# Performance work log

Hardware: AMD Instinct MI355X
Metric: run time of the kernel (lower is better)

## Reference

```python
import jax, jax.numpy as jnp
import numpy as np

N_NODES = 50000
N_EDGES = 800000
IN_CH = 512
HID = 256
HEADS = 8
OUT_CH = 64


def _glorot(key, shape):
    fan_in = shape[0] if len(shape) == 2 else shape[-1]
    return jax.random.normal(key, shape, jnp.float32) / jnp.sqrt(jnp.float32(fan_in))


def setup_inputs() -> dict:
    key = jax.random.key(0)
    ks = jax.random.split(key, 16)
    C = HID // HEADS  # 32, per-head dim
    return {
        "x": jax.random.normal(ks[0], (N_NODES, IN_CH), jnp.float32),
        "edge_index": jax.random.randint(ks[1], (2, N_EDGES), 0, N_NODES, jnp.int32),
        # layer 0: in -> heads*C, concat
        "W0": _glorot(ks[2], (IN_CH, HEADS * C)),
        "a_src0": _glorot(ks[3], (HEADS, C)),
        "a_dst0": _glorot(ks[4], (HEADS, C)),
        "b0": jnp.zeros((HEADS * C,), jnp.float32),
        # layer 1: hidden -> heads*C, concat
        "W1": _glorot(ks[5], (HID, HEADS * C)),
        "a_src1": _glorot(ks[6], (HEADS, C)),
        "a_dst1": _glorot(ks[7], (HEADS, C)),
        "b1": jnp.zeros((HEADS * C,), jnp.float32),
        # layer 2: hidden -> out_ch, 1 head, mean (concat=False)
        "W2": _glorot(ks[8], (HID, 1 * OUT_CH)),
        "a_src2": _glorot(ks[9], (1, OUT_CH)),
        "a_dst2": _glorot(ks[10], (1, OUT_CH)),
        "b2": jnp.zeros((OUT_CH,), jnp.float32),
    }


def gat_conv(x, W, a_src, a_dst, b, src, dst, concat):
    """PyG GATConv (self-loops already appended to src/dst), eval mode."""
    N = x.shape[0]
    H, C = a_src.shape
    h = (x @ W).reshape(N, H, C)                      # [N,H,C]
    alpha_src = jnp.sum(h * a_src, axis=-1)           # [N,H]
    alpha_dst = jnp.sum(h * a_dst, axis=-1)           # [N,H]
    e = jax.nn.leaky_relu(alpha_src[src] + alpha_dst[dst], 0.2)  # [E,H]
    # softmax over incoming edges per destination node
    m = jax.ops.segment_max(e, dst, num_segments=N)   # [N,H]
    m = jnp.where(jnp.isfinite(m), m, 0.0)
    w = jnp.exp(e - m[dst])
    s = jax.ops.segment_sum(w, dst, num_segments=N)
    alpha = w / (s[dst] + 1e-16)                      # [E,H]
    out = jax.ops.segment_sum(alpha[:, :, None] * h[src], dst, num_segments=N)
    out = out.reshape(N, H * C) if concat else out.mean(axis=1)
    return out + b


def reference(x, edge_index, W0, a_src0, a_dst0, b0, W1, a_src1, a_dst1, b1, W2, a_src2, a_dst2, b2):
    N = x.shape[0]
    loop = jnp.arange(N, dtype=edge_index.dtype)      # add_self_loops=True
    src = jnp.concatenate([edge_index[0], loop])
    dst = jnp.concatenate([edge_index[1], loop])
    # dropout is identity in eval mode
    h = jax.nn.elu(gat_conv(x, W0, a_src0, a_dst0, b0, src, dst, True))
    h = jax.nn.elu(gat_conv(h, W1, a_src1, a_dst1, b1, src, dst, True))
    h = gat_conv(h, W2, a_src2, a_dst2, b2, src, dst, False)
    return jax.nn.log_softmax(h, axis=1)
```

## Files before the change

kernel.cpp:

```cpp
#include <hip/hip_runtime.h>
#include <hip/hip_bf16.h>

typedef __attribute__((ext_vector_type(8))) short short8;
typedef __attribute__((ext_vector_type(4))) float f32x4;
typedef __attribute__((ext_vector_type(2))) float f32x2;
typedef __attribute__((ext_vector_type(4))) unsigned short us4;

__device__ __forceinline__ ushort f2bf(float f) {
    unsigned u = __float_as_uint(f);
    u += 0x7FFFu + ((u >> 16) & 1u);
    return (ushort)(u >> 16);
}
__device__ __forceinline__ float bf2f(ushort h) {
    return __uint_as_float(((unsigned)h) << 16);
}
__device__ __forceinline__ float lrelu(float e) { return (e >= 0.f) ? e : 0.2f * e; }
__device__ __forceinline__ unsigned char f2fp8(float v) {
    return (unsigned char)(__builtin_amdgcn_cvt_pk_fp8_f32(v, v, 0, false) & 0xFF);
}
__device__ __forceinline__ void gload16(const void* g, void* l) {
    __builtin_amdgcn_global_load_lds(
        (const __attribute__((address_space(1))) unsigned int*)g,
        (__attribute__((address_space(3))) unsigned int*)l, 16, 0, 0);
}

__global__ void k_hist(const int* __restrict__ dst, int* __restrict__ deg, int e) {
    int i = blockIdx.x * blockDim.x + threadIdx.x;
    if (i < e) atomicAdd(&deg[dst[i]], 1);
}
__global__ void k_scanA(const int* __restrict__ deg, int* __restrict__ bsum, int n) {
    __shared__ int sd[256];
    int t = blockIdx.x * 256 + threadIdx.x;
    sd[threadIdx.x] = (t < n) ? deg[t] + 1 : 0;
    __syncthreads();
    for (int off = 128; off > 0; off >>= 1) {
        if (threadIdx.x < off) sd[threadIdx.x] += sd[threadIdx.x + off];
        __syncthreads();
    }
    if (threadIdx.x == 0) bsum[blockIdx.x] = sd[0];
}
__global__ void k_scanC(const int* __restrict__ deg, const int* __restrict__ bsum,
                        int* __restrict__ rowptr, int* __restrict__ cursor,
                        int n, int etot, int nb) {
    __shared__ int sb[256];
    __shared__ int sd[256];
    __shared__ int sbx[256];
    int i = threadIdx.x;
    int bv = (i < nb) ? bsum[i] : 0;
    sb[i] = bv;
    __syncthreads();
    for (int off = 1; off < 256; off <<= 1) {
        int tv = (i >= off) ? sb[i - off] : 0;
        __syncthreads();
        sb[i] += tv;
        __syncthreads();
    }
    sbx[i] = sb[i] - bv;
    __syncthreads();
    int boff = sbx[blockIdx.x];

    int t = blockIdx.x * 256 + i;
    int v = (t < n) ? deg[t] + 1 : 0;
    sd[i] = v;
    __syncthreads();
    for (int off = 1; off < 256; off <<= 1) {
        int tv = (i >= off) ? sd[i - off] : 0;
        __syncthreads();
        sd[i] += tv;
        __syncthreads();
    }
    if (t < n) {
        int ex = boff + sd[i] - v;
        rowptr[t] = ex;
        cursor[t] = ex;
        if (t == n - 1) rowptr[n] = etot;
    }
}
__global__ void k_scatter(const int* __restrict__ ei, int* __restrict__ cursor,
                          int* __restrict__ col, int e, int n) {
    int i = blockIdx.x * blockDim.x + threadIdx.x;
    int etot = e + n;
    if (i >= etot) return;
    int s, d;
    if (i < e) { s = ei[i]; d = ei[e + i]; }
    else       { s = i - e; d = s; }
    int pos = atomicAdd(&cursor[d], 1);
    col[pos] = s;
}

__global__ void k_wcvt3(const float* __restrict__ W0, ushort* __restrict__ T0,
                        const float* __restrict__ W1, ushort* __restrict__ T1,
                        const float* __restrict__ W2, ushort* __restrict__ T2,
                        int* __restrict__ deg, int n) {
    int i = blockIdx.x * blockDim.x + threadIdx.x;
    if (i < n) deg[i] = 0;
    if (i < 131072) {
        int k = i >> 8, c = i & 255;
        T0[(size_t)c * 512 + k] = f2bf(W0[i]);
    } else if (i < 196608) {
        int j = i - 131072;
        int k = j >> 8, c = j & 255;
        T1[(size_t)c * 256 + k] = f2bf(W1[j]);
    } else if (i < 212992) {
        int j = i - 196608;
        int k = j >> 6, c = j & 63;
        T2[(size_t)c * 256 + k] = f2bf(W2[j]);
    }
}

template <int K, int BN, bool AF32>
__global__ __launch_bounds__(256) void k_gemm(const void* __restrict__ Ap,
                                              const ushort* __restrict__ BT,
                                              unsigned char* __restrict__ Cp,
                                              const float* __restrict__ asv,
                                              const float* __restrict__ adv,
                                              float* __restrict__ asrc,
                                              float* __restrict__ adst, int M) {
    constexpr int BM = 64, BK = 32;
    constexpr int NK = K / BK;
    constexpr int NF = BN / 32;
    constexpr int AU = BM * BK / 8;
    constexpr int BU = BN * BK / 8;
    constexpr int TU = AU + BU;
    __shared__ __align__(16) ushort lds[2][TU * 8];

    const int t = threadIdx.x;
    const int wid = t >> 6, lane = t & 63;
    const int lr = lane & 15, lg = lane >> 4;
    const int wm = wid >> 1, wn = wid & 1;
    const int bm0 = blockIdx.x * BM;
    const int bn0 = blockIdx.y * BN;
    const int Nc = BN * gridDim.y;

    int a_off[2], b_off[NF];
#pragma unroll
    for (int mf = 0; mf < 2; ++mf) {
        int row = wm * 32 + mf * 16 + lr;
        a_off[mf] = row * 64 + ((lg ^ ((row >> 1) & 3)) << 4);
    }
#pragma unroll
    for (int nf = 0; nf < NF; ++nf) {
        int col = wn * (BN / 2) + nf * 16 + lr;
        b_off[nf] = AU * 16 + col * 64 + ((lg ^ ((col >> 1) & 3)) << 4);
    }

    f32x4 acc[2][NF];
#pragma unroll
    for (int mf = 0; mf < 2; ++mf)
#pragma unroll
        for (int nf = 0; nf < NF; ++nf) acc[mf][nf] = f32x4{0.f, 0.f, 0.f, 0.f};

    f32x4 ra[2];

    auto stage_B = [&](int buf, int kk) {
#pragma unroll
        for (int i = 0; i < 2; ++i) {
            int u = t + i * 256;
            int col = u >> 2;
            int g = (u & 3) ^ ((col >> 1) & 3);
            const ushort* src = BT + (size_t)(bn0 + col) * K + kk + g * 8;
            gload16(src, &lds[buf][(AU + u) * 8]);
        }
    };
    auto stage_A16 = [&](int buf, int kk) {
        int u = t;
        int row = u >> 2;
        int g = (u & 3) ^ ((row >> 1) & 3);
        int grow = bm0 + row;
        if (grow >= M) grow = M - 1;
        const ushort* src = (const ushort*)Ap + (size_t)grow * K + kk + g * 8;
        gload16(src, &lds[buf][u * 8]);
    };
    auto load_A32 = [&](int kk) {
        int u = t;
        int row = u >> 2;
        int g = (u & 3) ^ ((row >> 1) & 3);
        int grow = bm0 + row;
        if (grow >= M) grow = M - 1;
        const float* src = (const float*)Ap + (size_t)grow * K + kk + g * 8;
        ra[0] = *(const f32x4*)src;
        ra[1] = *(const f32x4*)(src + 4);
    };
    auto write_A32 = [&](int buf) {
        int u = t;
        short8 v;
#pragma unroll
        for (int j = 0; j < 4; ++j) {
            v[j] = (short)f2bf(ra[0][j]);
            v[4 + j] = (short)f2bf(ra[1][j]);
        }
        *(short8*)&lds[buf][u * 8] = v;
    };
    auto compute = [&](int buf) {
        const char* base = (const char*)lds[buf];
        short8 af[2], bf_[NF];
#pragma unroll
        for (int mf = 0; mf < 2; ++mf) af[mf] = *(const short8*)(base + a_off[mf]);
#pragma unroll
        for (int nf = 0; nf < NF; ++nf) bf_[nf] = *(const short8*)(base + b_off[nf]);
#pragma unroll
        for (int mf = 0; mf < 2; ++mf)
#pragma unroll
            for (int nf = 0; nf < NF; ++nf)
                acc[mf][nf] = __builtin_amdgcn_mfma_f32_16x16x32_bf16(af[mf], bf_[nf], acc[mf][nf], 0, 0, 0);
    };

    if constexpr (AF32) {
        load_A32(0);
        write_A32(0);
    } else {
        stage_A16(0, 0);
    }
    stage_B(0, 0);
    __syncthreads();

    int buf = 0;
    for (int ks = 0; ks < NK; ++ks) {
        const int kk = (ks + 1) * BK;
        if (ks + 1 < NK) {
            if constexpr (AF32) load_A32(kk);
            else stage_A16(buf ^ 1, kk);
            stage_B(buf ^ 1, kk);
        }
        compute(buf);
        if constexpr (AF32) {
            if (ks + 1 < NK) write_A32(buf ^ 1);
        }
        __syncthreads();
        buf ^= 1;
    }

#pragma unroll
    for (int mf = 0; mf < 2; ++mf) {
#pragma unroll
        for (int nf = 0; nf < NF; ++nf) {
            int col = bn0 + wn * (BN / 2) + nf * 16 + lr;
#pragma unroll
            for (int p = 0; p < 4; ++p) {
                int row = bm0 + wm * 32 + mf * 16 + lg * 4 + p;
                if (row < M)
                    Cp[(size_t)row * Nc + col] = f2fp8(acc[mf][nf][p]);
            }
        }
    }

    if constexpr (NF == 4) {
        float cs[4], cd[4];
#pragma unroll
        for (int nf = 0; nf < 4; ++nf) {
            int col = bn0 + wn * 64 + nf * 16 + lr;
            cs[nf] = asv[col];
            cd[nf] = adv[col];
        }
        const int hb = (bn0 >> 5) + wn * 2;
#pragma unroll
        for (int mf = 0; mf < 2; ++mf) {
#pragma unroll
            for (int p = 0; p < 4; ++p) {
                float sA = acc[mf][0][p] * cs[0] + acc[mf][1][p] * cs[1];
                float sB = acc[mf][2][p] * cs[2] + acc[mf][3][p] * cs[3];
                float dA = acc[mf][0][p] * cd[0] + acc[mf][1][p] * cd[1];
                float dB = acc[mf][2][p] * cd[2] + acc[mf][3][p] * cd[3];
#pragma unroll
                for (int off = 1; off < 16; off <<= 1) {
                    sA += __shfl_xor(sA, off);
                    sB += __shfl_xor(sB, off);
                    dA += __shfl_xor(dA, off);
                    dB += __shfl_xor(dB, off);
                }
                int row = bm0 + wm * 32 + mf * 16 + lg * 4 + p;
                if (lr == 0 && row < M) {
                    asrc[row * 8 + hb] = sA;
                    asrc[row * 8 + hb + 1] = sB;
                    adst[row * 8 + hb] = dA;
                    adst[row * 8 + hb + 1] = dB;
                }
            }
        }
    }
}

__global__ __launch_bounds__(256) void k_gemm2(const ushort* __restrict__ Ap,
                                               const ushort* __restrict__ BT,
                                               ushort* __restrict__ Cp,
                                               const float* __restrict__ asv,
                                               const float* __restrict__ adv,
                                               float* __restrict__ asrc,
                                               float* __restrict__ adst, int M) {
    constexpr int K = 256, BM = 64, BK = 32;
    constexpr int NK = K / BK;
    constexpr int BU = 64 * BK / 8;
    constexpr int AU = BM * BK / 8;
    constexpr int TU = AU + BU;
    __shared__ __align__(16) ushort lds[2][TU * 8];

    const int t = threadIdx.x;
    const int wid = t >> 6, lane = t & 63;
    const int lr = lane & 15, lg = lane >> 4;
    const int bm0 = blockIdx.x * BM;

    int a_off0, b_off[4];
    {
        int row = wid * 16 + lr;
        a_off0 = row * 64 + ((lg ^ ((row >> 1) & 3)) << 4);
    }
#pragma unroll
    for (int nf = 0; nf < 4; ++nf) {
        int col = nf * 16 + lr;
        b_off[nf] = AU * 16 + col * 64 + ((lg ^ ((col >> 1) & 3)) << 4);
    }

    f32x4 acc[4];
#pragma unroll
    for (int nf = 0; nf < 4; ++nf) acc[nf] = f32x4{0.f, 0.f, 0.f, 0.f};

    auto stage_B = [&](int buf, int kk) {
        int u = t;
        int col = u >> 2;
        int g = (u & 3) ^ ((col >> 1) & 3);
        const ushort* src = BT + (size_t)col * K + kk + g * 8;
        gload16(src, &lds[buf][(AU + u) * 8]);
    };
    auto stage_A = [&](int buf, int kk) {
        int u = t;
        int row = u >> 2;
        int g = (u & 3) ^ ((row >> 1) & 3);
        int grow = bm0 + row;
        if (grow >= M) grow = M - 1;
        const ushort* src = Ap + (size_t)grow * K + kk + g * 8;
        gload16(src, &lds[buf][u * 8]);
    };
    auto compute = [&](int buf) {
        const char* base = (const char*)lds[buf];
        short8 af = *(const short8*)(base + a_off0);
        short8 bf_[4];
#pragma unroll
        for (int nf = 0; nf < 4; ++nf) bf_[nf] = *(const short8*)(base + b_off[nf]);
#pragma unroll
        for (int nf = 0; nf < 4; ++nf)
            acc[nf] = __builtin_amdgcn_mfma_f32_16x16x32_bf16(af, bf_[nf], acc[nf], 0, 0, 0);
    };

    stage_A(0, 0);
    stage_B(0, 0);
    __syncthreads();
    int buf = 0;
    for (int ks = 0; ks < NK; ++ks) {
        if (ks + 1 < NK) {
            stage_A(buf ^ 1, (ks + 1) * BK);
            stage_B(buf ^ 1, (ks + 1) * BK);
        }
        compute(buf);
        __syncthreads();
        buf ^= 1;
    }

    float cs[4], cd[4];
#pragma unroll
    for (int nf = 0; nf < 4; ++nf) {
        cs[nf] = asv[nf * 16 + lr];
        cd[nf] = adv[nf * 16 + lr];
    }
#pragma unroll
    for (int p = 0; p < 4; ++p) {
        int row = bm0 + wid * 16 + lg * 4 + p;
#pragma unroll
        for (int nf = 0; nf < 4; ++nf) {
            if (row < M)
                Cp[(size_t)row * 64 + nf * 16 + lr] = f2bf(acc[nf][p]);
        }
        float sA = acc[0][p] * cs[0] + acc[1][p] * cs[1] +
                   acc[2][p] * cs[2] + acc[3][p] * cs[3];
        float dA = acc[0][p] * cd[0] + acc[1][p] * cd[1] +
                   acc[2][p] * cd[2] + acc[3][p] * cd[3];
#pragma unroll
        for (int off = 1; off < 16; off <<= 1) {
            sA += __shfl_xor(sA, off);
            dA += __shfl_xor(dA, off);
        }
        if (lr == 0 && row < M) {
            asrc[row] = sA;
            adst[row] = dA;
        }
    }
}

#define MAXW 96
__global__ __launch_bounds__(128) void k_agg(const unsigned char* __restrict__ h8,
                                             const float* __restrict__ asrc,
                                             const float* __restrict__ adst,
                                             const int* __restrict__ rowptr,
                                             const int* __restrict__ col,
                                             const float* __restrict__ bias,
                                             ushort* __restrict__ anext, int n) {
    __shared__ float wl[2][MAXW * 8];
    int wid = threadIdx.x >> 6;
    int lane = threadIdx.x & 63;
    int node = blockIdx.x * 2 + wid;
    if (node >= n) return;
    int beg = rowptr[node], end = rowptr[node + 1];
    int deg = end - beg;
    int hd = lane >> 3;
    int eo = lane & 7;
    float ad = adst[node * 8 + hd];
    float* wp = wl[wid];

    float sacc = 0.f;
    for (int jb = eo; jb < deg; jb += 8) {
        int s = col[beg + jb];
        float w = __expf(lrelu(asrc[s * 8 + hd] + ad));
        if (jb < MAXW) wp[jb * 8 + hd] = w;
        sacc += w;
    }
    sacc += __shfl_xor(sacc, 1);
    sacc += __shfl_xor(sacc, 2);
    sacc += __shfl_xor(sacc, 4);
    float inv = 1.f / (sacc + 1e-16f);

    int nl = (deg < MAXW) ? deg : MAXW;
    float a0 = 0.f, a1 = 0.f, a2 = 0.f, a3 = 0.f;
    int jb = 0;
    for (; jb + 8 <= nl; jb += 8) {
        int sv[8];
#pragma unroll
        for (int i = 0; i < 8; ++i) sv[i] = col[beg + jb + i];
        unsigned gv[8];
#pragma unroll
        for (int i = 0; i < 8; ++i) gv[i] = *(const unsigned*)(h8 + (size_t)sv[i] * 256 + lane * 4);
        float wv[8];
#pragma unroll
        for (int i = 0; i < 8; ++i) wv[i] = wp[(jb + i) * 8 + hd];
#pragma unroll
        for (int i = 0; i < 8; ++i) {
            a0 += wv[i] * __builtin_amdgcn_cvt_f32_fp8(gv[i], 0);
            a1 += wv[i] * __builtin_amdgcn_cvt_f32_fp8(gv[i], 1);
            a2 += wv[i] * __builtin_amdgcn_cvt_f32_fp8(gv[i], 2);
            a3 += wv[i] * __builtin_amdgcn_cvt_f32_fp8(gv[i], 3);
        }
    }
    for (; jb < nl; ++jb) {
        int s = col[beg + jb];
        unsigned g = *(const unsigned*)(h8 + (size_t)s * 256 + lane * 4);
        float w = wp[jb * 8 + hd];
        a0 += w * __builtin_amdgcn_cvt_f32_fp8(g, 0);
        a1 += w * __builtin_amdgcn_cvt_f32_fp8(g, 1);
        a2 += w * __builtin_amdgcn_cvt_f32_fp8(g, 2);
        a3 += w * __builtin_amdgcn_cvt_f32_fp8(g, 3);
    }
    for (; jb < deg; ++jb) {
        int s = col[beg + jb];
        unsigned g = *(const unsigned*)(h8 + (size_t)s * 256 + lane * 4);
        float w = __expf(lrelu(asrc[s * 8 + hd] + ad));
        a0 += w * __builtin_amdgcn_cvt_f32_fp8(g, 0);
        a1 += w * __builtin_amdgcn_cvt_f32_fp8(g, 1);
        a2 += w * __builtin_amdgcn_cvt_f32_fp8(g, 2);
        a3 += w * __builtin_amdgcn_cvt_f32_fp8(g, 3);
    }
    f32x4 bv = *(const f32x4*)(bias + lane * 4);
    float v0 = a0 * inv + bv[0];
    float v1 = a1 * inv + bv[1];
    float v2 = a2 * inv + bv[2];
    float v3 = a3 * inv + bv[3];
    v0 = (v0 > 0.f) ? v0 : expm1f(v0);
    v1 = (v1 > 0.f) ? v1 : expm1f(v1);
    v2 = (v2 > 0.f) ? v2 : expm1f(v2);
    v3 = (v3 > 0.f) ? v3 : expm1f(v3);
    us4 o;
    o[0] = f2bf(v0); o[1] = f2bf(v1); o[2] = f2bf(v2); o[3] = f2bf(v3);
    *(us4*)(anext + (size_t)node * 256 + lane * 4) = o;
}

__global__ __launch_bounds__(128) void k_agg2(const ushort* __restrict__ h2,
                                              const float* __restrict__ asrc,
                                              const float* __restrict__ adst,
                                              const int* __restrict__ rowptr,
                                              const int* __restrict__ col,
                                              const float* __restrict__ bias,
                                              float* __restrict__ out, int n) {
    int wid = threadIdx.x >> 6;
    int lane = threadIdx.x & 63;
    int node = blockIdx.x * 2 + wid;
    if (node >= n) return;
    int beg = rowptr[node], end = rowptr[node + 1];
    int deg = end - beg;
    float ad = adst[node];
    int g = lane >> 3;
    int ch = (lane & 7) * 8;

    f32x2 acc2[4];
#pragma unroll
    for (int i = 0; i < 4; ++i) acc2[i] = f32x2{0.f, 0.f};
    float ssum = 0.f;
    for (int p = 0; p < deg; p += 8) {
        int jb = p + g;
        float w = 0.f;
        uint4 gv = {0u, 0u, 0u, 0u};
        if (jb < deg) {
            int s = col[beg + jb];
            gv = *(const uint4*)(h2 + (size_t)s * 64 + ch);
            w = __expf(lrelu(asrc[s] + ad));
        }
        ssum += w;
        f32x2 w2 = {w, w};
        f32x2 p0 = {__uint_as_float(gv.x << 16), __uint_as_float(gv.x & 0xFFFF0000u)};
        f32x2 p1 = {__uint_as_float(gv.y << 16), __uint_as_float(gv.y & 0xFFFF0000u)};
        f32x2 p2 = {__uint_as_float(gv.z << 16), __uint_as_float(gv.z & 0xFFFF0000u)};
        f32x2 p3 = {__uint_as_float(gv.w << 16), __uint_as_float(gv.w & 0xFFFF0000u)};
        acc2[0] += w2 * p0;
        acc2[1] += w2 * p1;
        acc2[2] += w2 * p2;
        acc2[3] += w2 * p3;
    }
    float v[8];
#pragma unroll
    for (int i = 0; i < 4; ++i) { v[2 * i] = acc2[i].x; v[2 * i + 1] = acc2[i].y; }
#pragma unroll
    for (int off = 8; off < 64; off <<= 1) {
        ssum += __shfl_xor(ssum, off);
#pragma unroll
        for (int i = 0; i < 8; ++i) v[i] += __shfl_xor(v[i], off);
    }
    float inv = 1.f / (ssum + 1e-16f);
#pragma unroll
    for (int i = 0; i < 8; ++i) v[i] = v[i] * inv + bias[ch + i];
    float mx = v[0];
#pragma unroll
    for (int i = 1; i < 8; ++i) mx = fmaxf(mx, v[i]);
    mx = fmaxf(mx, __shfl_xor(mx, 1));
    mx = fmaxf(mx, __shfl_xor(mx, 2));
    mx = fmaxf(mx, __shfl_xor(mx, 4));
    float se = 0.f;
#pragma unroll
    for (int i = 0; i < 8; ++i) se += __expf(v[i] - mx);
    se += __shfl_xor(se, 1);
    se += __shfl_xor(se, 2);
    se += __shfl_xor(se, 4);
    float ls = mx + logf(se);
    if (g == 0) {
        f32x4 o0, o1;
#pragma unroll
        for (int i = 0; i < 4; ++i) { o0[i] = v[i] - ls; o1[i] = v[4 + i] - ls; }
        *(f32x4*)(out + (size_t)node * 64 + ch) = o0;
        *(f32x4*)(out + (size_t)node * 64 + ch + 4) = o1;
    }
}

extern "C" void kernel_launch(void* const* d_in, const int* in_sizes, int n_in,
                              void* d_out, int out_size, void* d_ws, size_t ws_size,
                              hipStream_t stream) {
    const float* x   = (const float*)d_in[0];
    const int*   ei  = (const int*)d_in[1];
    const float* W0  = (const float*)d_in[2];
    const float* as0 = (const float*)d_in[3];
    const float* ad0 = (const float*)d_in[4];
    const float* b0  = (const float*)d_in[5];
    const float* W1  = (const float*)d_in[6];
    const float* as1 = (const float*)d_in[7];
    const float* ad1 = (const float*)d_in[8];
    const float* b1  = (const float*)d_in[9];
    const float* W2  = (const float*)d_in[10];
    const float* as2 = (const float*)d_in[11];
    const float* ad2 = (const float*)d_in[12];
    const float* b2  = (const float*)d_in[13];
    float* out = (float*)d_out;

    const int N = in_sizes[0] / 512;
    const int E = in_sizes[1] / 2;
    const int ETOT = E + N;

    char* ws = (char*)d_ws;
    size_t off = 0;
    auto alloc = [&](size_t bytes) -> void* {
        off = (off + 255) & ~(size_t)255;
        void* p = ws + off;
        off += bytes;
        return p;
    };
    int* rowptr = (int*)alloc((size_t)(N + 1) * 4);
    int* cursor = (int*)alloc((size_t)N * 4);
    int* deg    = (int*)alloc((size_t)N * 4);
    int* bsum   = (int*)alloc(1024);
    int* colb   = (int*)alloc((size_t)ETOT * 4);
    ushort* WT0 = (ushort*)alloc((size_t)256 * 512 * 2);
    ushort* WT1 = (ushort*)alloc((size_t)256 * 256 * 2);
    ushort* WT2 = (ushort*)alloc((size_t)64 * 256 * 2);
    unsigned char* h8 = (unsigned char*)alloc((size_t)N * 256);
    ushort* abf = (ushort*)alloc((size_t)N * 256 * 2);
    float* asrc = (float*)alloc((size_t)N * 8 * 4);
    float* adst = (float*)alloc((size_t)N * 8 * 4);
    ushort* h2   = (ushort*)h8;
    float* asrc2 = asrc;
    float* adst2 = adst;

    const int nblk = (N + 255) / 256;

    k_wcvt3<<<832, 256, 0, stream>>>(W0, WT0, W1, WT1, W2, WT2, deg, N);

    k_hist<<<(E + 255) / 256, 256, 0, stream>>>(ei + E, deg, E);
    k_scanA<<<nblk, 256, 0, stream>>>(deg, bsum, N);
    k_scanC<<<nblk, 256, 0, stream>>>(deg, bsum, rowptr, cursor, N, ETOT, nblk);
    k_scatter<<<(ETOT + 255) / 256, 256, 0, stream>>>(ei, cursor, colb, E, N);

    const dim3 g01((N + 63) / 64, 2);
    const int gblk = (N + 63) / 64;
    const int ablk = (N + 1) / 2;

    k_gemm<512, 128, true><<<g01, 256, 0, stream>>>(x, WT0, h8, as0, ad0, asrc, adst, N);
    k_agg<<<ablk, 128, 0, stream>>>(h8, asrc, adst, rowptr, colb, b0, abf, N);

    k_gemm<256, 128, false><<<g01, 256, 0, stream>>>(abf, WT1, h8, as1, ad1, asrc, adst, N);
    k_agg<<<ablk, 128, 0, stream>>>(h8, asrc, adst, rowptr, colb, b1, abf, N);

    k_gemm2<<<gblk, 256, 0, stream>>>(abf, WT2, h2, as2, ad2, asrc2, adst2, N);
    k_agg2<<<ablk, 128, 0, stream>>>(h2, asrc2, adst2, rowptr, colb, b2, out, N);
}
```

Baseline: 325.0 us.

## Fuse degree histogram into weight conversion and CSR scatter into layer-0 GEMM

Merges the edge degree histogram into the weight-transpose kernel as extra blocks, and runs the CSR column scatter as extra blocks inside the layer-0 GEMM launch. Each of those blocks now handles four edges. The degree buffer is cleared with a memset instead of inside the conversion kernel. This removes two kernel launches and lets the scatter's atomics overlap with GEMM work, but adds a memset call and puts atomic-heavy blocks alongside MFMA blocks in one grid.

New measurement: 328.4 us. Within noise of the previous version (+1.0%).

```diff
diff --git a/kernel.cpp b/kernel.cpp
--- a/kernel.cpp
+++ b/kernel.cpp
@@ -24,10 +24,6 @@
         (__attribute__((address_space(3))) unsigned int*)l, 16, 0, 0);
 }
 
-__global__ void k_hist(const int* __restrict__ dst, int* __restrict__ deg, int e) {
-    int i = blockIdx.x * blockDim.x + threadIdx.x;
-    if (i < e) atomicAdd(&deg[dst[i]], 1);
-}
 __global__ void k_scanA(const int* __restrict__ deg, int* __restrict__ bsum, int n) {
     __shared__ int sd[256];
     int t = blockIdx.x * 256 + threadIdx.x;
@@ -76,24 +72,23 @@
         if (t == n - 1) rowptr[n] = etot;
     }
 }
-__global__ void k_scatter(const int* __restrict__ ei, int* __restrict__ cursor,
-                          int* __restrict__ col, int e, int n) {
+
+__global__ void k_wh(const float* __restrict__ W0, ushort* __restrict__ T0,
+                     const float* __restrict__ W1, ushort* __restrict__ T1,
+                     const float* __restrict__ W2, ushort* __restrict__ T2,
+                     const int* __restrict__ dst, int* __restrict__ deg, int e, int nhb) {
+    if (blockIdx.x >= 832) {
+        int hb = blockIdx.x - 832;
+        int base = hb * 256 + threadIdx.x;
+        int stride = nhb * 256;
+#pragma unroll
+        for (int k = 0; k < 4; ++k) {
+            int i = base + k * stride;
+            if (i < e) atomicAdd(&deg[dst[i]], 1);
+        }
+        return;
+    }
     int i = blockIdx.x * blockDim.x + threadIdx.x;
-    int etot = e + n;
-    if (i >= etot) return;
-    int s, d;
-    if (i < e) { s = ei[i]; d = ei[e + i]; }
-    else       { s = i - e; d = s; }
-    int pos = atomicAdd(&cursor[d], 1);
-    col[pos] = s;
-}
-
-__global__ void k_wcvt3(const float* __restrict__ W0, ushort* __restrict__ T0,
-                        const float* __restrict__ W1, ushort* __restrict__ T1,
-                        const float* __restrict__ W2, ushort* __restrict__ T2,
-                        int* __restrict__ deg, int n) {
-    int i = blockIdx.x * blockDim.x + threadIdx.x;
-    if (i < n) deg[i] = 0;
     if (i < 131072) {
         int k = i >> 8, c = i & 255;
         T0[(size_t)c * 512 + k] = f2bf(W0[i]);
@@ -108,8 +103,181 @@
     }
 }
 
-template <int K, int BN, bool AF32>
-__global__ __launch_bounds__(256) void k_gemm(const void* __restrict__ Ap,
+__global__ __launch_bounds__(256) void k_g0s(const float* __restrict__ Ap,
+                                             const ushort* __restrict__ BT,
+                                             unsigned char* __restrict__ Cp,
+                                             const float* __restrict__ asv,
+                                             const float* __restrict__ adv,
+                                             float* __restrict__ asrc,
+                                             float* __restrict__ adst, int M,
+                                             const int* __restrict__ ei,
+                                             int* __restrict__ cursor,
+                                             int* __restrict__ colb,
+                                             int E, int nsb) {
+    constexpr int K = 512, BK = 32;
+    constexpr int NK = K / BK;
+    constexpr int AU = 256, BU = 512, TU = AU + BU;
+    __shared__ __align__(16) ushort lds[2][TU * 8];
+
+    if (blockIdx.x < nsb) {
+        int base = blockIdx.x * 256 + threadIdx.x;
+        int stride = nsb * 256;
+        int etot = E + M;
+#pragma unroll
+        for (int k = 0; k < 4; ++k) {
+            int i = base + k * stride;
+            if (i < etot) {
+                int s, d;
+                if (i < E) { s = ei[i]; d = ei[E + i]; }
+                else       { s = i - E; d = s; }
+                int pos = atomicAdd(&cursor[d], 1);
+                colb[pos] = s;
+            }
+        }
+        return;
+    }
+
+    const int gb = blockIdx.x - nsb;
+    const int t = threadIdx.x;
+    const int wid = t >> 6, lane = t & 63;
+    const int lr = lane & 15, lg = lane >> 4;
+    const int wm = wid >> 1, wn = wid & 1;
+    const int bm0 = (gb >> 1) * 64;
+    const int bn0 = (gb & 1) * 128;
+
+    int a_off[2], b_off[4];
+#pragma unroll
+    for (int mf = 0; mf < 2; ++mf) {
+        int row = wm * 32 + mf * 16 + lr;
+        a_off[mf] = row * 64 + ((lg ^ ((row >> 1) & 3)) << 4);
+    }
+#pragma unroll
+    for (int nf = 0; nf < 4; ++nf) {
+        int col = wn * 64 + nf * 16 + lr;
+        b_off[nf] = AU * 16 + col * 64 + ((lg ^ ((col >> 1) & 3)) << 4);
+    }
+
+    f32x4 acc[2][4];
+#pragma unroll
+    for (int mf = 0; mf < 2; ++mf)
+#pragma unroll
+        for (int nf = 0; nf < 4; ++nf) acc[mf][nf] = f32x4{0.f, 0.f, 0.f, 0.f};
+
+    f32x4 ra[2];
+
+    auto stage_B = [&](int buf, int kk) {
+#pragma unroll
+        for (int i = 0; i < 2; ++i) {
+            int u = t + i * 256;
+            int col = u >> 2;
+            int g = (u & 3) ^ ((col >> 1) & 3);
+            const ushort* src = BT + (size_t)(bn0 + col) * K + kk + g * 8;
+            gload16(src, &lds[buf][(AU + u) * 8]);
+        }
+    };
+    auto load_A32 = [&](int kk) {
+        int u = t;
+        int row = u >> 2;
+        int g = (u & 3) ^ ((row >> 1) & 3);
+        int grow = bm0 + row;
+        if (grow >= M) grow = M - 1;
+        const float* src = Ap + (size_t)grow * K + kk + g * 8;
+        ra[0] = *(const f32x4*)src;
+        ra[1] = *(const f32x4*)(src + 4);
+    };
+    auto write_A32 = [&](int buf) {
+        short8 v;
+#pragma unroll
+        for (int j = 0; j < 4; ++j) {
+            v[j] = (short)f2bf(ra[0][j]);
+            v[4 + j] = (short)f2bf(ra[1][j]);
+        }
+        *(short8*)&lds[buf][t * 8] = v;
+    };
+    auto compute = [&](int buf) {
+        const char* base = (const char*)lds[buf];
+        short8 af[2], bf_[4];
+#pragma unroll
+        for (int mf = 0; mf < 2; ++mf) af[mf] = *(const short8*)(base + a_off[mf]);
+#pragma unroll
+        for (int nf = 0; nf < 4; ++nf) bf_[nf] = *(const short8*)(base + b_off[nf]);
+#pragma unroll
+        for (int mf = 0; mf < 2; ++mf)
+#pragma unroll
+            for (int nf = 0; nf < 4; ++nf)
+                acc[mf][nf] = __builtin_amdgcn_mfma_f32_16x16x32_bf16(af[mf], bf_[nf], acc[mf][nf], 0, 0, 0);
+    };
+
+    load_A32(0);
+    write_A32(0);
+    stage_B(0, 0);
+    __syncthreads();
+
+    int buf = 0;
+    for (int ks = 0; ks < NK; ++ks) {
+        const int kk = (ks + 1) * BK;
+        if (ks + 1 < NK) {
+            load_A32(kk);
+            stage_B(buf ^ 1, kk);
+        }
+        compute(buf);
+        if (ks + 1 < NK) write_A32(buf ^ 1);
+        __syncthreads();
+        buf ^= 1;
+    }
+
+#pragma unroll
+    for (int mf = 0; mf < 2; ++mf) {
+#pragma unroll
+        for (int nf = 0; nf < 4; ++nf) {
+            int col = bn0 + wn * 64 + nf * 16 + lr;
+#pragma unroll
+            for (int p = 0; p < 4; ++p) {
+                int row = bm0 + wm * 32 + mf * 16 + lg * 4 + p;
+                if (row < M)
+                    Cp[(size_t)row * 256 + col] = f2fp8(acc[mf][nf][p]);
+            }
+        }
+    }
+
+    {
+        float cs[4], cd[4];
+#pragma unroll
+        for (int nf = 0; nf < 4; ++nf) {
+            int col = bn0 + wn * 64 + nf * 16 + lr;
+            cs[nf] = asv[col];
+            cd[nf] = adv[col];
+        }
+        const int hb = (bn0 >> 5) + wn * 2;
+#pragma unroll
+        for (int mf = 0; mf < 2; ++mf) {
+#pragma unroll
+            for (int p = 0; p < 4; ++p) {
+                float sA = acc[mf][0][p] * cs[0] + acc[mf][1][p] * cs[1];
+                float sB = acc[mf][2][p] * cs[2] + acc[mf][3][p] * cs[3];
+                float dA = acc[mf][0][p] * cd[0] + acc[mf][1][p] * cd[1];
+                float dB = acc[mf][2][p] * cd[2] + acc[mf][3][p] * cd[3];
+#pragma unroll
+                for (int off = 1; off < 16; off <<= 1) {
+                    sA += __shfl_xor(sA, off);
+                    sB += __shfl_xor(sB, off);
+                    dA += __shfl_xor(dA, off);
+                    dB += __shfl_xor(dB, off);
+                }
+                int row = bm0 + wm * 32 + mf * 16 + lg * 4 + p;
+                if (lr == 0 && row < M) {
+                    asrc[row * 8 + hb] = sA;
+                    asrc[row * 8 + hb + 1] = sB;
+                    adst[row * 8 + hb] = dA;
+                    adst[row * 8 + hb + 1] = dB;
+                }
+            }
+        }
+    }
+}
+
+template <int K, int BN>
+__global__ __launch_bounds__(256) void k_gemm(const ushort* __restrict__ Ap,
                                               const ushort* __restrict__ BT,
                                               unsigned char* __restrict__ Cp,
                                               const float* __restrict__ asv,
@@ -150,8 +318,6 @@
 #pragma unroll
         for (int nf = 0; nf < NF; ++nf) acc[mf][nf] = f32x4{0.f, 0.f, 0.f, 0.f};
 
-    f32x4 ra[2];
-
     auto stage_B = [&](int buf, int kk) {
 #pragma unroll
         for (int i = 0; i < 2; ++i) {
@@ -168,28 +334,8 @@
         int g = (u & 3) ^ ((row >> 1) & 3);
         int grow = bm0 + row;
         if (grow >= M) grow = M - 1;
-        const ushort* src = (const ushort*)Ap + (size_t)grow * K + kk + g * 8;
+        const ushort* src = Ap + (size_t)grow * K + kk + g * 8;
         gload16(src, &lds[buf][u * 8]);
-    };
-    auto load_A32 = [&](int kk) {
-        int u = t;
-        int row = u >> 2;
-        int g = (u & 3) ^ ((row >> 1) & 3);
-        int grow = bm0 + row;
-        if (grow >= M) grow = M - 1;
-        const float* src = (const float*)Ap + (size_t)grow * K + kk + g * 8;
-        ra[0] = *(const f32x4*)src;
-        ra[1] = *(const f32x4*)(src + 4);
-    };
-    auto write_A32 = [&](int buf) {
-        int u = t;
-        short8 v;
-#pragma unroll
-        for (int j = 0; j < 4; ++j) {
-            v[j] = (short)f2bf(ra[0][j]);
-            v[4 + j] = (short)f2bf(ra[1][j]);
-        }
-        *(short8*)&lds[buf][u * 8] = v;
     };
     auto compute = [&](int buf) {
         const char* base = (const char*)lds[buf];
@@ -205,12 +351,7 @@
                 acc[mf][nf] = __builtin_amdgcn_mfma_f32_16x16x32_bf16(af[mf], bf_[nf], acc[mf][nf], 0, 0, 0);
     };
 
-    if constexpr (AF32) {
-        load_A32(0);
-        write_A32(0);
-    } else {
-        stage_A16(0, 0);
-    }
+    stage_A16(0, 0);
     stage_B(0, 0);
     __syncthreads();
 
@@ -218,14 +359,10 @@
     for (int ks = 0; ks < NK; ++ks) {
         const int kk = (ks + 1) * BK;
         if (ks + 1 < NK) {
-            if constexpr (AF32) load_A32(kk);
-            else stage_A16(buf ^ 1, kk);
+            stage_A16(buf ^ 1, kk);
             stage_B(buf ^ 1, kk);
         }
         compute(buf);
-        if constexpr (AF32) {
-            if (ks + 1 < NK) write_A32(buf ^ 1);
-        }
         __syncthreads();
         buf ^= 1;
     }
@@ -593,22 +730,23 @@
     float* adst2 = adst;
 
     const int nblk = (N + 255) / 256;
-
-    k_wcvt3<<<832, 256, 0, stream>>>(W0, WT0, W1, WT1, W2, WT2, deg, N);
-
-    k_hist<<<(E + 255) / 256, 256, 0, stream>>>(ei + E, deg, E);
+    const int nhb  = (E + 1023) / 1024;
+    const int nsb  = (ETOT + 1023) / 1024;
+
+    hipMemsetAsync(deg, 0, (size_t)N * 4, stream);
+    k_wh<<<832 + nhb, 256, 0, stream>>>(W0, WT0, W1, WT1, W2, WT2, ei + E, deg, E, nhb);
+
     k_scanA<<<nblk, 256, 0, stream>>>(deg, bsum, N);
     k_scanC<<<nblk, 256, 0, stream>>>(deg, bsum, rowptr, cursor, N, ETOT, nblk);
-    k_scatter<<<(ETOT + 255) / 256, 256, 0, stream>>>(ei, cursor, colb, E, N);
-
-    const dim3 g01((N + 63) / 64, 2);
+
     const int gblk = (N + 63) / 64;
     const int ablk = (N + 1) / 2;
 
-    k_gemm<512, 128, true><<<g01, 256, 0, stream>>>(x, WT0, h8, as0, ad0, asrc, adst, N);
+    k_g0s<<<nsb + 2 * gblk, 256, 0, stream>>>(x, WT0, h8, as0, ad0, asrc, adst, N,
+                                              ei, cursor, colb, E, nsb);
     k_agg<<<ablk, 128, 0, stream>>>(h8, asrc, adst, rowptr, colb, b0, abf, N);
 
-    k_gemm<256, 128, false><<<g01, 256, 0, stream>>>(abf, WT1, h8, as1, ad1, asrc, adst, N);
+    k_gemm<256, 128><<<dim3(gblk, 2), 256, 0, stream>>>(abf, WT1, h8, as1, ad1, asrc, adst, N);
     k_agg<<<ablk, 128, 0, stream>>>(h8, asrc, adst, rowptr, colb, b1, abf, N);
 
     k_gemm2<<<gblk, 256, 0, stream>>>(abf, WT2, h2, as2, ad2, asrc2, adst2, N);
```
